# Performance work log

Measured on AMD Instinct MI355X. Metric: run time of the kernel, lower is better.

The kernel has to match this reference:

```python
import jax, jax.numpy as jnp
import numpy as np

N_NODES = 50000


def gcn_conv(h, W, b, src, dst, n_nodes):
    # PyG GCNConv: h' = D^{-1/2} (A + I) D^{-1/2} (h @ W) + b
    h = h @ W  # [N, out]
    deg = jax.ops.segment_sum(jnp.ones_like(dst, dtype=h.dtype), dst, num_segments=n_nodes)
    dinv = jnp.where(deg > 0, jax.lax.rsqrt(deg), 0.0)  # [N]
    norm = dinv[src] * dinv[dst]  # [E]
    msg = h[src] * norm[:, None]  # [E, out]
    out = jax.ops.segment_sum(msg, dst, num_segments=n_nodes)
    return out + b


def setup_inputs() -> dict:
    key = jax.random.key(0)
    ks = jax.random.split(key, 12)
    N, E, P, D, H = N_NODES, 1600000, 200000, 128, 128
    s = lambda fan_in: 1.0 / np.sqrt(fan_in)
    return {
        "x": jax.random.normal(ks[0], (N, D), dtype=jnp.float32),
        "edge_index": jax.random.randint(ks[1], (2, E), 0, N, dtype=jnp.int32),
        "drug_pairs": jax.random.randint(ks[2], (P, 2), 0, N, dtype=jnp.int32),
        "W1": jax.random.normal(ks[3], (D, H), dtype=jnp.float32) * s(D),
        "b1": jnp.zeros((H,), dtype=jnp.float32),
        "W2": jax.random.normal(ks[4], (H, H), dtype=jnp.float32) * s(H),
        "b2": jnp.zeros((H,), dtype=jnp.float32),
        "Wh1": jax.random.normal(ks[5], (2 * H, H), dtype=jnp.float32) * s(2 * H),
        "bh1": jnp.zeros((H,), dtype=jnp.float32),
        "Wh2": jax.random.normal(ks[6], (H, 1), dtype=jnp.float32) * s(H),
        "bh2": jnp.zeros((1,), dtype=jnp.float32),
    }


def reference(x, edge_index, drug_pairs, W1, b1, W2, b2, Wh1, bh1, Wh2, bh2):
    n = x.shape[0]
    # add self-loops once (GCNConv default add_self_loops=True)
    loop = jnp.arange(n, dtype=edge_index.dtype)
    src = jnp.concatenate([edge_index[0], loop])
    dst = jnp.concatenate([edge_index[1], loop])

    h = jax.nn.relu(gcn_conv(x, W1, b1, src, dst, n))  # dropout = identity (eval)
    h = jax.nn.relu(gcn_conv(h, W2, b2, src, dst, n))

    combined = jnp.concatenate([h[drug_pairs[:, 0]], h[drug_pairs[:, 1]]], axis=1)  # [P, 2H]
    out = jax.nn.relu(combined @ Wh1 + bh1) @ Wh2 + bh2  # [P, 1]
    return out
```

## Files before the change

### kernel.cpp

```cpp
#include <hip/hip_runtime.h>
#include <hip/hip_fp16.h>


#define BSH 9
#define BSZ (1 << BSH)
#define MSB 4096
#define XPAD 132
#define HB 256

typedef __attribute__((ext_vector_type(8))) short bf16x8;
typedef __attribute__((ext_vector_type(8))) _Float16 f16x8;
typedef __attribute__((ext_vector_type(4))) float f32x4;

__device__ __forceinline__ void acc8(uint4 u, float4& lo, float4& hi) {
  float2 f0 = __half22float2(((const __half2*)&u)[0]);
  float2 f1 = __half22float2(((const __half2*)&u)[1]);
  float2 f2 = __half22float2(((const __half2*)&u)[2]);
  float2 f3 = __half22float2(((const __half2*)&u)[3]);
  lo.x += f0.x; lo.y += f0.y; lo.z += f1.x; lo.w += f1.y;
  hi.x += f2.x; hi.y += f2.y; hi.z += f3.x; hi.w += f3.y;
}

__device__ __forceinline__ void split8(const float* v, bf16x8& hi, bf16x8& lo) {
#pragma unroll
  for (int j = 0; j < 8; ++j) {
    unsigned u = __float_as_uint(v[j]);
    hi[j] = (short)(u >> 16);
    float lf = v[j] - __uint_as_float(u & 0xffff0000u);
    lo[j] = (short)(__float_as_uint(lf) >> 16);
  }
}

__global__ __launch_bounds__(256) void k_prep_hist(
    const float* __restrict__ W1, const float* __restrict__ W2,
    const float* __restrict__ Wh1, short* __restrict__ fragH,
    short* __restrict__ fragL,
    const int* __restrict__ dst, int* __restrict__ gcnt, int e, int kb) {
  if (blockIdx.x >= 32) {
    __shared__ int h4[512];
    int bid = blockIdx.x - 32;
    int tid = threadIdx.x, wid = tid >> 6;
    for (int t = tid; t < 512; t += 256) h4[t] = 0;
    __syncthreads();
    for (int i = bid * 256 + tid; i < e; i += HB * 256) {
      int d = __builtin_nontemporal_load(&dst[i]);
      atomicAdd(&h4[wid * 128 + (d >> BSH)], 1);
    }
    __syncthreads();
    if (tid < kb)
      atomicAdd(&gcnt[tid], h4[tid] + h4[128 + tid] + h4[256 + tid] + h4[384 + tid]);
    return;
  }
  int g = blockIdx.x * 256 + threadIdx.x;
  int w = g >> 11;
  int rem = g & 2047;
  int lane = rem & 63;
  int ts = rem >> 6;
  int t = ts >> 2, s = ts & 3;
  int n = (t << 4) + (lane & 15);
  int k0 = s * 32 + (lane >> 4) * 8;
  const float* W = (w == 0) ? W1 : (w == 1) ? W2 : (w == 2) ? Wh1 : (Wh1 + 128 * 128);
  short h[8], l[8];
#pragma unroll
  for (int j = 0; j < 8; ++j) {
    float x = W[(k0 + j) * 128 + n];
    if (w == 0) {
      unsigned u = __float_as_uint(x);
      h[j] = (short)(u >> 16);
      float lf = x - __uint_as_float(u & 0xffff0000u);
      l[j] = (short)(__float_as_uint(lf) >> 16);
    } else {
      __half hh = __float2half(x);
      h[j] = __half_as_short(hh);
      l[j] = __half_as_short(__float2half(x - __half2float(hh)));
    }
  }
  ((int4*)fragH)[g] = *(int4*)h;
  ((int4*)fragL)[g] = *(int4*)l;
}

__device__ __forceinline__ void gemm1_body(
    const float* __restrict__ X, const short* __restrict__ fragH,
    const short* __restrict__ fragL, __half* __restrict__ C16, int n,
    int bid, float* sX) {
  int tid = threadIdx.x;
  int row0 = bid * 64;
  const float2* X2 = (const float2*)(X + (size_t)row0 * 128);
#pragma unroll
  for (int it = 0; it < 16; ++it) {
    int t = it * 256 + tid;
    int r = t >> 6, c2 = t & 63;
    int gr = row0 + r;
    float2 v = (gr < n) ? X2[t] : make_float2(0.f, 0.f);
    *(float2*)&sX[r * XPAD + c2 * 2] = v;
  }
  __syncthreads();
  int wid = tid >> 6, lane = tid & 63;
  int r0 = row0 + wid * 16;
  if (r0 >= n) return;
  int m = lane & 15, quad = lane >> 4;
  const float* xrow = sX + (wid * 16 + m) * XPAD;
  f32x4 acc[8];
#pragma unroll
  for (int t = 0; t < 8; ++t) acc[t] = (f32x4)(0.f);
  const int4* FH = (const int4*)fragH;
  const int4* FL = (const int4*)fragL;
#pragma unroll
  for (int s = 0; s < 4; ++s) {
    int k0 = s * 32 + quad * 8;
    float xv[8];
    *(float2*)&xv[0] = *(const float2*)(xrow + k0);
    *(float2*)&xv[2] = *(const float2*)(xrow + k0 + 2);
    *(float2*)&xv[4] = *(const float2*)(xrow + k0 + 4);
    *(float2*)&xv[6] = *(const float2*)(xrow + k0 + 6);
    bf16x8 ah, al;
    split8(xv, ah, al);
#pragma unroll
    for (int t = 0; t < 8; ++t) {
      int idx = (t * 4 + s) * 64 + lane;
      bf16x8 bh = *(const bf16x8*)&FH[idx];
      bf16x8 bl = *(const bf16x8*)&FL[idx];
      acc[t] = __builtin_amdgcn_mfma_f32_16x16x32_bf16(ah, bh, acc[t], 0, 0, 0);
      acc[t] = __builtin_amdgcn_mfma_f32_16x16x32_bf16(al, bh, acc[t], 0, 0, 0);
      acc[t] = __builtin_amdgcn_mfma_f32_16x16x32_bf16(ah, bl, acc[t], 0, 0, 0);
    }
  }
#pragma unroll
  for (int t = 0; t < 8; ++t) {
#pragma unroll
    for (int r = 0; r < 4; ++r) {
      int row = r0 + quad * 4 + r;
      C16[(size_t)row * 128 + t * 16 + m] = __float2half(acc[t][r]);
    }
  }
}

__device__ __forceinline__ void multisplit_body(
    const int* __restrict__ src, const int* __restrict__ dst,
    const int* __restrict__ gcnt, int* __restrict__ gcur,
    int* __restrict__ tmp, int e, int kb, int bid, int* lds) {
  int* h4 = lds;
  int* off = lds + 512;
  int* sbase = lds + 1024;
  int* ws = lds + 1152;
  int tid = threadIdx.x, wid = tid >> 6, lane = tid & 63;
  for (int t = tid; t < 512; t += 256) h4[t] = 0;
  __syncthreads();
  int i0 = bid * MSB + tid;
  int d[16], rk[16];
#pragma unroll
  for (int u = 0; u < 16; ++u) {
    int i = i0 + u * 256;
    if (i < e) {
      d[u] = __builtin_nontemporal_load(&dst[i]);
      rk[u] = atomicAdd(&h4[wid * 128 + (d[u] >> BSH)], 1);
    }
  }
  __syncthreads();
  int tot = 0;
  if (tid < 128) {
    int c0 = h4[tid], c1 = h4[128 + tid], c2 = h4[256 + tid], c3 = h4[384 + tid];
    off[tid] = 0; off[128 + tid] = c0;
    off[256 + tid] = c0 + c1; off[384 + tid] = c0 + c1 + c2;
    tot = c0 + c1 + c2 + c3;
  }
  int v = (tid < 128 && tid < kb) ? gcnt[tid] : 0;
  int orig = v;
#pragma unroll
  for (int o = 1; o < 64; o <<= 1) {
    int u = __shfl_up(v, o, 64);
    if (lane >= o) v += u;
  }
  if (lane == 63 && wid < 2) ws[wid] = v;
  __syncthreads();
  if (tid < 128) sbase[tid] = ((wid == 1) ? ws[0] : 0) + v - orig;
  __syncthreads();
  if (tid < kb && tot > 0) sbase[tid] += atomicAdd(&gcur[tid], tot);
  __syncthreads();
#pragma unroll
  for (int u = 0; u < 16; ++u) {
    int i = i0 + u * 256;
    if (i < e) {
      int s = __builtin_nontemporal_load(&src[i]);
      int k = d[u] >> BSH;
      tmp[sbase[k] + off[wid * 128 + k] + rk[u]] = ((d[u] & (BSZ - 1)) << 16) | s;
    }
  }
}

__global__ __launch_bounds__(256) void k_ms_gemm1(
    const int* __restrict__ src, const int* __restrict__ dst,
    const int* __restrict__ gcnt, int* __restrict__ gcur,
    int* __restrict__ tmp, int e, int kb, int msblocks,
    const float* __restrict__ X, const short* __restrict__ fragH,
    const short* __restrict__ fragL, __half* __restrict__ C16, int n) {
  __shared__ float sX[64 * XPAD];
  if ((int)blockIdx.x < msblocks) {
    multisplit_body(src, dst, gcnt, gcur, tmp, e, kb, blockIdx.x, (int*)sX);
    return;
  }
  gemm1_body(X, fragH, fragL, C16, n, blockIdx.x - msblocks, sX);
}

__global__ __launch_bounds__(512) void k_bucket_build(
    const int* __restrict__ tmp, const int* __restrict__ gcnt,
    int* __restrict__ rowptr, float* __restrict__ dinv,
    unsigned short* __restrict__ colarr, int n, int kb, int e) {
  __shared__ int dl[BSZ], cl[BSZ], sbase[128], ws[8];
  int t = threadIdx.x, b = blockIdx.x;
  int lane = t & 63, w = t >> 6;
  int v = (t < 128 && t < kb) ? gcnt[t] : 0;
  int orig0 = v;
#pragma unroll
  for (int o = 1; o < 64; o <<= 1) {
    int u = __shfl_up(v, o, 64);
    if (lane >= o) v += u;
  }
  if (lane == 63 && w < 2) ws[w] = v;
  dl[t] = 0;
  __syncthreads();
  if (t < 128) sbase[t] = ((w == 1) ? ws[0] : 0) + v - orig0;
  __syncthreads();
  int s0 = sbase[b];
  int s1 = s0 + gcnt[b];
  for (int j = s0 + t; j < s1; j += 512)
    atomicAdd(&dl[((unsigned)tmp[j]) >> 16], 1);
  __syncthreads();
  int dv = dl[t], orig = dv;
#pragma unroll
  for (int o = 1; o < 64; o <<= 1) {
    int u = __shfl_up(dv, o, 64);
    if (lane >= o) dv += u;
  }
  if (lane == 63) ws[w] = dv;
  __syncthreads();
  if (t == 0) {
    int a = 0;
#pragma unroll
    for (int k = 0; k < 8; ++k) { int x = ws[k]; ws[k] = a; a += x; }
  }
  __syncthreads();
  int ex = ws[w] + dv - orig;
  cl[t] = ex;
  int node = (b << BSH) + t;
  if (node < n) {
    rowptr[node] = s0 + ex;
    dinv[node] = rsqrtf((float)(orig + 1));
  }
  if (b == kb - 1 && t == 0) rowptr[n] = e;
  __syncthreads();
  for (int j = s0 + t; j < s1; j += 512) {
    int p = tmp[j];
    int r = atomicAdd(&cl[((unsigned)p) >> 16], 1);
    colarr[s0 + r] = (unsigned short)(p & 0xFFFF);
  }
}

__global__ __launch_bounds__(256) void k_gscale(__half* __restrict__ g16,
                                                const float* __restrict__ dinv,
                                                int n) {
  int idx = blockIdx.x * 256 + threadIdx.x;
  if (idx >= n * 16) return;
  float di = dinv[idx >> 4];
  uint4 u = ((const uint4*)g16)[idx];
  __half2* hp = (__half2*)&u;
#pragma unroll
  for (int k = 0; k < 4; ++k) {
    float2 f = __half22float2(hp[k]);
    hp[k] = __floats2half2_rn(f.x * di, f.y * di);
  }
  ((uint4*)g16)[idx] = u;
}

__global__ __launch_bounds__(256) void k_gemm_f16(
    const __half* __restrict__ X16, const short* __restrict__ fragH,
    const short* __restrict__ fragL, const float* __restrict__ rowscale,
    __half* __restrict__ C16, int n) {
  int wid = threadIdx.x >> 6, lane = threadIdx.x & 63;
  int r0 = (blockIdx.x * 4 + wid) * 16;
  if (r0 >= n) return;
  int m = lane & 15, quad = lane >> 4;
  const uint4* Xr = (const uint4*)(X16 + (size_t)(r0 + m) * 128);
  f32x4 acc[8];
#pragma unroll
  for (int t = 0; t < 8; ++t) acc[t] = (f32x4)(0.f);
  const int4* FH = (const int4*)fragH;
  const int4* FL = (const int4*)fragL;
#pragma unroll
  for (int s = 0; s < 4; ++s) {
    uint4 av = Xr[quad + 4 * s];
    f16x8 a = *(const f16x8*)&av;
#pragma unroll
    for (int t = 0; t < 8; ++t) {
      int idx = (t * 4 + s) * 64 + lane;
      int4 bhv = FH[idx], blv = FL[idx];
      f16x8 bh = *(const f16x8*)&bhv;
      f16x8 bl = *(const f16x8*)&blv;
      acc[t] = __builtin_amdgcn_mfma_f32_16x16x32_f16(a, bh, acc[t], 0, 0, 0);
      acc[t] = __builtin_amdgcn_mfma_f32_16x16x32_f16(a, bl, acc[t], 0, 0, 0);
    }
  }
  float sc[4];
#pragma unroll
  for (int r = 0; r < 4; ++r)
    sc[r] = rowscale ? rowscale[r0 + quad * 4 + r] : 1.f;
#pragma unroll
  for (int t = 0; t < 8; ++t) {
#pragma unroll
    for (int r = 0; r < 4; ++r) {
      int row = r0 + quad * 4 + r;
      C16[(size_t)row * 128 + t * 16 + m] = __float2half(acc[t][r] * sc[r]);
    }
  }
}

__global__ __launch_bounds__(256) void k_gemm_dual_f16(
    const __half* __restrict__ X16,
    const short* __restrict__ fHa, const short* __restrict__ fLa,
    const short* __restrict__ fHb, const short* __restrict__ fLb,
    __half* __restrict__ A16, __half* __restrict__ B16, int n) {
  int wid = threadIdx.x >> 6, lane = threadIdx.x & 63;
  int r0 = (blockIdx.x * 4 + wid) * 16;
  if (r0 >= n) return;
  int m = lane & 15, quad = lane >> 4;
  const uint4* Xr = (const uint4*)(X16 + (size_t)(r0 + m) * 128);
  f32x4 accA[8], accB[8];
#pragma unroll
  for (int t = 0; t < 8; ++t) { accA[t] = (f32x4)(0.f); accB[t] = (f32x4)(0.f); }
  const int4* FHa = (const int4*)fHa; const int4* FLa = (const int4*)fLa;
  const int4* FHb = (const int4*)fHb; const int4* FLb = (const int4*)fLb;
#pragma unroll
  for (int s = 0; s < 4; ++s) {
    uint4 av = Xr[quad + 4 * s];
    f16x8 a = *(const f16x8*)&av;
#pragma unroll
    for (int t = 0; t < 8; ++t) {
      int idx = (t * 4 + s) * 64 + lane;
      int4 v0 = FHa[idx], v1 = FLa[idx], v2 = FHb[idx], v3 = FLb[idx];
      accA[t] = __builtin_amdgcn_mfma_f32_16x16x32_f16(a, *(const f16x8*)&v0, accA[t], 0, 0, 0);
      accA[t] = __builtin_amdgcn_mfma_f32_16x16x32_f16(a, *(const f16x8*)&v1, accA[t], 0, 0, 0);
      accB[t] = __builtin_amdgcn_mfma_f32_16x16x32_f16(a, *(const f16x8*)&v2, accB[t], 0, 0, 0);
      accB[t] = __builtin_amdgcn_mfma_f32_16x16x32_f16(a, *(const f16x8*)&v3, accB[t], 0, 0, 0);
    }
  }
#pragma unroll
  for (int t = 0; t < 8; ++t) {
#pragma unroll
    for (int r = 0; r < 4; ++r) {
      int row = r0 + quad * 4 + r;
      A16[(size_t)row * 128 + t * 16 + m] = __float2half(accA[t][r]);
      B16[(size_t)row * 128 + t * 16 + m] = __float2half(accB[t][r]);
    }
  }
}

__global__ __launch_bounds__(256) void k_agg_h(
    const __half2* __restrict__ g2, const float* __restrict__ dinv,
    const int* __restrict__ rowptr, const unsigned short* __restrict__ col,
    const float* __restrict__ bias, __half* __restrict__ out16, int n) {
  int i = blockIdx.x * 4 + (threadIdx.x >> 6);
  if (i >= n) return;
  int lane = threadIdx.x & 63;
  int sub = lane >> 4;
  int c8 = lane & 15;
  const uint4* G = (const uint4*)g2;
  float4 z = make_float4(0.f, 0.f, 0.f, 0.f);
  float4 lo0 = z, lo1 = z, lo2 = z, lo3 = z, hi0 = z, hi1 = z, hi2 = z, hi3 = z;
  if (sub == 0) acc8(G[(size_t)i * 16 + c8], lo0, hi0);
  int beg = rowptr[i], end = rowptr[i + 1];
  int j = beg;
  for (; j + 16 <= end; j += 16) {
    int s0 = __builtin_nontemporal_load(&col[j + sub]);
    int s1 = __builtin_nontemporal_load(&col[j + 4 + sub]);
    int s2 = __builtin_nontemporal_load(&col[j + 8 + sub]);
    int s3 = __builtin_nontemporal_load(&col[j + 12 + sub]);
    uint4 u0 = G[(size_t)s0 * 16 + c8];
    uint4 u1 = G[(size_t)s1 * 16 + c8];
    uint4 u2 = G[(size_t)s2 * 16 + c8];
    uint4 u3 = G[(size_t)s3 * 16 + c8];
    acc8(u0, lo0, hi0); acc8(u1, lo1, hi1);
    acc8(u2, lo2, hi2); acc8(u3, lo3, hi3);
  }
  for (; j + 4 <= end; j += 4) {
    int s0 = __builtin_nontemporal_load(&col[j + sub]);
    acc8(G[(size_t)s0 * 16 + c8], lo1, hi1);
  }
  int rem = end - j;
  if (sub < rem) {
    int s0 = __builtin_nontemporal_load(&col[j + sub]);
    acc8(G[(size_t)s0 * 16 + c8], lo2, hi2);
  }
  float4 lo, hi;
  lo.x = (lo0.x + lo1.x) + (lo2.x + lo3.x);
  lo.y = (lo0.y + lo1.y) + (lo2.y + lo3.y);
  lo.z = (lo0.z + lo1.z) + (lo2.z + lo3.z);
  lo.w = (lo0.w + lo1.w) + (lo2.w + lo3.w);
  hi.x = (hi0.x + hi1.x) + (hi2.x + hi3.x);
  hi.y = (hi0.y + hi1.y) + (hi2.y + hi3.y);
  hi.z = (hi0.z + hi1.z) + (hi2.z + hi3.z);
  hi.w = (hi0.w + hi1.w) + (hi2.w + hi3.w);
  lo.x += __shfl_down(lo.x, 32, 64); lo.x += __shfl_down(lo.x, 16, 64);
  lo.y += __shfl_down(lo.y, 32, 64); lo.y += __shfl_down(lo.y, 16, 64);
  lo.z += __shfl_down(lo.z, 32, 64); lo.z += __shfl_down(lo.z, 16, 64);
  lo.w += __shfl_down(lo.w, 32, 64); lo.w += __shfl_down(lo.w, 16, 64);
  hi.x += __shfl_down(hi.x, 32, 64); hi.x += __shfl_down(hi.x, 16, 64);
  hi.y += __shfl_down(hi.y, 32, 64); hi.y += __shfl_down(hi.y, 16, 64);
  hi.z += __shfl_down(hi.z, 32, 64); hi.z += __shfl_down(hi.z, 16, 64);
  hi.w += __shfl_down(hi.w, 32, 64); hi.w += __shfl_down(hi.w, 16, 64);
  if (sub == 0) {
    float di = dinv[i];
    float4 b0 = ((const float4*)bias)[2 * c8];
    float4 b1 = ((const float4*)bias)[2 * c8 + 1];
    __half2 q0 = __floats2half2_rn(fmaxf(fmaf(di, lo.x, b0.x), 0.f),
                                   fmaxf(fmaf(di, lo.y, b0.y), 0.f));
    __half2 q1 = __floats2half2_rn(fmaxf(fmaf(di, lo.z, b0.z), 0.f),
                                   fmaxf(fmaf(di, lo.w, b0.w), 0.f));
    __half2 q2 = __floats2half2_rn(fmaxf(fmaf(di, hi.x, b1.x), 0.f),
                                   fmaxf(fmaf(di, hi.y, b1.y), 0.f));
    __half2 q3 = __floats2half2_rn(fmaxf(fmaf(di, hi.z, b1.z), 0.f),
                                   fmaxf(fmaf(di, hi.w, b1.w), 0.f));
    uint4 o;
    o.x = *(unsigned*)&q0; o.y = *(unsigned*)&q1;
    o.z = *(unsigned*)&q2; o.w = *(unsigned*)&q3;
    ((uint4*)out16)[(size_t)i * 16 + c8] = o;
  }
}

__global__ __launch_bounds__(256) void k_pairs_h(
    const __half* __restrict__ A, const __half* __restrict__ B,
    const int* __restrict__ pairs, const float* __restrict__ bh1,
    const float* __restrict__ wh2, const float* __restrict__ bh2,
    float* __restrict__ out, int P) {
  int wp = (blockIdx.x * 4 + (threadIdx.x >> 6)) * 4;
  int lane = threadIdx.x & 63;
  int sub = lane >> 4;
  int c8 = lane & 15;
  int pr = sub >> 1;
  int ab = sub & 1;
  const uint4* T = ab ? (const uint4*)B : (const uint4*)A;
  int pA = wp + pr;
  int pB = wp + 2 + pr;
  uint4 u0 = make_uint4(0, 0, 0, 0), u1 = u0;
  if (pA < P) {
    int r = pairs[2 * pA + ab];
    u0 = T[(size_t)r * 16 + c8];
  }
  if (pB < P) {
    int r = pairs[2 * pB + ab];
    u1 = T[(size_t)r * 16 + c8];
  }
  float4 b0 = ((const float4*)bh1)[2 * c8];
  float4 b1 = ((const float4*)bh1)[2 * c8 + 1];
  float4 w0 = ((const float4*)wh2)[2 * c8];
  float4 w1 = ((const float4*)wh2)[2 * c8 + 1];
  float s0, s1;
  {
    float4 lo = make_float4(0, 0, 0, 0), hi = lo;
    acc8(u0, lo, hi);
    lo.x += __shfl_down(lo.x, 16, 64); lo.y += __shfl_down(lo.y, 16, 64);
    lo.z += __shfl_down(lo.z, 16, 64); lo.w += __shfl_down(lo.w, 16, 64);
    hi.x += __shfl_down(hi.x, 16, 64); hi.y += __shfl_down(hi.y, 16, 64);
    hi.z += __shfl_down(hi.z, 16, 64); hi.w += __shfl_down(hi.w, 16, 64);
    s0 = fmaxf(lo.x + b0.x, 0.f) * w0.x + fmaxf(lo.y + b0.y, 0.f) * w0.y +
         fmaxf(lo.z + b0.z, 0.f) * w0.z + fmaxf(lo.w + b0.w, 0.f) * w0.w +
         fmaxf(hi.x + b1.x, 0.f) * w1.x + fmaxf(hi.y + b1.y, 0.f) * w1.y +
         fmaxf(hi.z + b1.z, 0.f) * w1.z + fmaxf(hi.w + b1.w, 0.f) * w1.w;
  }
  {
    float4 lo = make_float4(0, 0, 0, 0), hi = lo;
    acc8(u1, lo, hi);
    lo.x += __shfl_down(lo.x, 16, 64); lo.y += __shfl_down(lo.y, 16, 64);
    lo.z += __shfl_down(lo.z, 16, 64); lo.w += __shfl_down(lo.w, 16, 64);
    hi.x += __shfl_down(hi.x, 16, 64); hi.y += __shfl_down(hi.y, 16, 64);
    hi.z += __shfl_down(hi.z, 16, 64); hi.w += __shfl_down(hi.w, 16, 64);
    s1 = fmaxf(lo.x + b0.x, 0.f) * w0.x + fmaxf(lo.y + b0.y, 0.f) * w0.y +
         fmaxf(lo.z + b0.z, 0.f) * w0.z + fmaxf(lo.w + b0.w, 0.f) * w0.w +
         fmaxf(hi.x + b1.x, 0.f) * w1.x + fmaxf(hi.y + b1.y, 0.f) * w1.y +
         fmaxf(hi.z + b1.z, 0.f) * w1.z + fmaxf(hi.w + b1.w, 0.f) * w1.w;
  }
#pragma unroll
  for (int o = 8; o > 0; o >>= 1) {
    s0 += __shfl_down(s0, o, 64);
    s1 += __shfl_down(s1, o, 64);
  }
  float bb = bh2[0];
  if (lane == 0 && wp < P) out[wp] = s0 + bb;
  if (lane == 32 && wp + 1 < P) out[wp + 1] = s0 + bb;
  if (lane == 0 && wp + 2 < P) out[wp + 2] = s1 + bb;
  if (lane == 32 && wp + 3 < P) out[wp + 3] = s1 + bb;
}

extern "C" void kernel_launch(void* const* d_in, const int* in_sizes, int n_in,
                              void* d_out, int out_size, void* d_ws, size_t ws_size,
                              hipStream_t stream) {
  const float* x   = (const float*)d_in[0];
  const int* ei    = (const int*)d_in[1];
  const int* pairs = (const int*)d_in[2];
  const float* W1  = (const float*)d_in[3];
  const float* b1  = (const float*)d_in[4];
  const float* W2  = (const float*)d_in[5];
  const float* b2  = (const float*)d_in[6];
  const float* Wh1 = (const float*)d_in[7];
  const float* bh1 = (const float*)d_in[8];
  const float* Wh2 = (const float*)d_in[9];
  const float* bh2 = (const float*)d_in[10];
  (void)n_in; (void)out_size; (void)ws_size;

  int N = in_sizes[0] / 128;
  int E = in_sizes[1] / 2;
  int P = in_sizes[2] / 2;
  const int* src = ei;
  const int* dst = ei + E;
  int KB = (N + BSZ - 1) >> BSH;

  char* wsp = (char*)d_ws;
  size_t off = 0;
  auto alloc = [&](size_t bytes) -> void* {
    void* p = wsp + off;
    off += (bytes + 255) & ~(size_t)255;
    return p;
  };
  __half* g16 = (__half*)alloc((size_t)N * 128 * 2);
  __half* h1  = (__half*)alloc((size_t)N * 128 * 2);
  __half* h2  = (__half*)alloc((size_t)N * 128 * 2);
  float* dinv = (float*)alloc((size_t)N * 4);
  int* rowptr = (int*)alloc((size_t)(N + 1) * 4);
  unsigned short* colarr = (unsigned short*)alloc((size_t)E * 2);
  int* tmp    = (int*)alloc((size_t)E * 4);
  short* fragH = (short*)alloc(4 * 2048 * 8 * 2);
  short* fragL = (short*)alloc(4 * 2048 * 8 * 2);
  int* gc     = (int*)alloc(2 * 128 * 4);
  int* gcnt = gc;
  int* gcur = gc + 128;
  __half* A16 = g16;
  __half* B16 = h1;
  short* fH_W1 = fragH + 0 * 16384;  short* fL_W1 = fragL + 0 * 16384;
  short* fH_W2 = fragH + 1 * 16384;  short* fL_W2 = fragL + 1 * 16384;
  short* fH_Wa = fragH + 2 * 16384;  short* fL_Wa = fragL + 2 * 16384;
  short* fH_Wb = fragH + 3 * 16384;  short* fL_Wb = fragL + 3 * 16384;

  int GB = (N + 63) / 64;
  int GF = (N / 16 + 3) / 4;
  int AB = (N + 3) / 4;
  int MS = (E + MSB - 1) / MSB;

  hipMemsetAsync(gc, 0, 2 * 128 * 4, stream);
  k_prep_hist<<<32 + HB, 256, 0, stream>>>(W1, W2, Wh1, fragH, fragL,
                                           dst, gcnt, E, KB);
  k_ms_gemm1<<<MS + GB, 256, 0, stream>>>(src, dst, gcnt, gcur, tmp, E, KB, MS,
                                          x, fH_W1, fL_W1, g16, N);
  k_bucket_build<<<KB, 512, 0, stream>>>(tmp, gcnt, rowptr, dinv, colarr, N, KB, E);
  k_gscale<<<(N * 16 + 255) / 256, 256, 0, stream>>>(g16, dinv, N);
  k_agg_h<<<AB, 256, 0, stream>>>((const __half2*)g16, dinv, rowptr, colarr, b1, h1, N);
  k_gemm_f16<<<GF, 256, 0, stream>>>(h1, fH_W2, fL_W2, dinv, g16, N);
  k_agg_h<<<AB, 256, 0, stream>>>((const __half2*)g16, dinv, rowptr, colarr, b2, h2, N);
  k_gemm_dual_f16<<<GF, 256, 0, stream>>>(h2, fH_Wa, fL_Wa, fH_Wb, fL_Wb,
                                          A16, B16, N);
  k_pairs_h<<<(P + 15) / 16, 256, 0, stream>>>(A16, B16, pairs, bh1, Wh2, bh2,
                                               (float*)d_out, P);
}
```

Baseline: 344.9 us.

## Fuse row scaling into bucket build and unroll histogram loops

Removes the separate k_gscale launch by applying the dinv scaling of g16 inside k_bucket_build, using per-block degree values kept in shared memory. The dst histogram now reads four ints per vector load with a 2x unrolled stride. The bucket count and scatter loops are unrolled 8x so more independent loads are in flight. This saves one launch and one global read of dinv, but the 98-block bucket kernel now also carries the whole g16 scaling pass, which may serialize work that was previously spread across many blocks.

```diff
diff --git a/kernel.cpp b/kernel.cpp
--- a/kernel.cpp
+++ b/kernel.cpp
@@ -11,6 +11,7 @@
 typedef __attribute__((ext_vector_type(8))) short bf16x8;
 typedef __attribute__((ext_vector_type(8))) _Float16 f16x8;
 typedef __attribute__((ext_vector_type(4))) float f32x4;
+typedef __attribute__((ext_vector_type(4))) int i32x4;
 
 __device__ __forceinline__ void acc8(uint4 u, float4& lo, float4& hi) {
   float2 f0 = __half22float2(((const __half2*)&u)[0]);
@@ -42,8 +43,31 @@
     int tid = threadIdx.x, wid = tid >> 6;
     for (int t = tid; t < 512; t += 256) h4[t] = 0;
     __syncthreads();
-    for (int i = bid * 256 + tid; i < e; i += HB * 256) {
-      int d = __builtin_nontemporal_load(&dst[i]);
+    const i32x4* dst4 = (const i32x4*)dst;
+    int ne4 = e >> 2;
+    const int STR = HB * 256;
+    int i = bid * 256 + tid;
+    for (; i < ne4 - STR; i += 2 * STR) {
+      i32x4 a = __builtin_nontemporal_load(&dst4[i]);
+      i32x4 b = __builtin_nontemporal_load(&dst4[i + STR]);
+      atomicAdd(&h4[wid * 128 + (a.x >> BSH)], 1);
+      atomicAdd(&h4[wid * 128 + (a.y >> BSH)], 1);
+      atomicAdd(&h4[wid * 128 + (a.z >> BSH)], 1);
+      atomicAdd(&h4[wid * 128 + (a.w >> BSH)], 1);
+      atomicAdd(&h4[wid * 128 + (b.x >> BSH)], 1);
+      atomicAdd(&h4[wid * 128 + (b.y >> BSH)], 1);
+      atomicAdd(&h4[wid * 128 + (b.z >> BSH)], 1);
+      atomicAdd(&h4[wid * 128 + (b.w >> BSH)], 1);
+    }
+    for (; i < ne4; i += STR) {
+      i32x4 a = __builtin_nontemporal_load(&dst4[i]);
+      atomicAdd(&h4[wid * 128 + (a.x >> BSH)], 1);
+      atomicAdd(&h4[wid * 128 + (a.y >> BSH)], 1);
+      atomicAdd(&h4[wid * 128 + (a.z >> BSH)], 1);
+      atomicAdd(&h4[wid * 128 + (a.w >> BSH)], 1);
+    }
+    if (bid == 0 && tid < (e & 3)) {
+      int d = dst[(ne4 << 2) + tid];
       atomicAdd(&h4[wid * 128 + (d >> BSH)], 1);
     }
     __syncthreads();
@@ -205,8 +229,10 @@
 __global__ __launch_bounds__(512) void k_bucket_build(
     const int* __restrict__ tmp, const int* __restrict__ gcnt,
     int* __restrict__ rowptr, float* __restrict__ dinv,
-    unsigned short* __restrict__ colarr, int n, int kb, int e) {
+    unsigned short* __restrict__ colarr, __half* __restrict__ g16,
+    int n, int kb, int e) {
   __shared__ int dl[BSZ], cl[BSZ], sbase[128], ws[8];
+  __shared__ float sdi[BSZ];
   int t = threadIdx.x, b = blockIdx.x;
   int lane = t & 63, w = t >> 6;
   int v = (t < 128 && t < kb) ? gcnt[t] : 0;
@@ -223,8 +249,29 @@
   __syncthreads();
   int s0 = sbase[b];
   int s1 = s0 + gcnt[b];
-  for (int j = s0 + t; j < s1; j += 512)
-    atomicAdd(&dl[((unsigned)tmp[j]) >> 16], 1);
+  {
+    int j = s0 + t;
+    for (; j < s1 - 3584; j += 4096) {
+      int v0 = tmp[j];
+      int v1 = tmp[j + 512];
+      int v2 = tmp[j + 1024];
+      int v3 = tmp[j + 1536];
+      int v4 = tmp[j + 2048];
+      int v5 = tmp[j + 2560];
+      int v6 = tmp[j + 3072];
+      int v7 = tmp[j + 3584];
+      atomicAdd(&dl[((unsigned)v0) >> 16], 1);
+      atomicAdd(&dl[((unsigned)v1) >> 16], 1);
+      atomicAdd(&dl[((unsigned)v2) >> 16], 1);
+      atomicAdd(&dl[((unsigned)v3) >> 16], 1);
+      atomicAdd(&dl[((unsigned)v4) >> 16], 1);
+      atomicAdd(&dl[((unsigned)v5) >> 16], 1);
+      atomicAdd(&dl[((unsigned)v6) >> 16], 1);
+      atomicAdd(&dl[((unsigned)v7) >> 16], 1);
+    }
+    for (; j < s1; j += 512)
+      atomicAdd(&dl[((unsigned)tmp[j]) >> 16], 1);
+  }
   __syncthreads();
   int dv = dl[t], orig = dv;
 #pragma unroll
@@ -243,33 +290,67 @@
   int ex = ws[w] + dv - orig;
   cl[t] = ex;
   int node = (b << BSH) + t;
+  float di = rsqrtf((float)(orig + 1));
+  sdi[t] = di;
   if (node < n) {
     rowptr[node] = s0 + ex;
-    dinv[node] = rsqrtf((float)(orig + 1));
+    dinv[node] = di;
   }
   if (b == kb - 1 && t == 0) rowptr[n] = e;
   __syncthreads();
-  for (int j = s0 + t; j < s1; j += 512) {
-    int p = tmp[j];
-    int r = atomicAdd(&cl[((unsigned)p) >> 16], 1);
-    colarr[s0 + r] = (unsigned short)(p & 0xFFFF);
-  }
-}
-
-__global__ __launch_bounds__(256) void k_gscale(__half* __restrict__ g16,
-                                                const float* __restrict__ dinv,
-                                                int n) {
-  int idx = blockIdx.x * 256 + threadIdx.x;
-  if (idx >= n * 16) return;
-  float di = dinv[idx >> 4];
-  uint4 u = ((const uint4*)g16)[idx];
-  __half2* hp = (__half2*)&u;
-#pragma unroll
-  for (int k = 0; k < 4; ++k) {
-    float2 f = __half22float2(hp[k]);
-    hp[k] = __floats2half2_rn(f.x * di, f.y * di);
-  }
-  ((uint4*)g16)[idx] = u;
+  {
+    int j = s0 + t;
+    for (; j < s1 - 3584; j += 4096) {
+      int p0 = tmp[j];
+      int p1 = tmp[j + 512];
+      int p2 = tmp[j + 1024];
+      int p3 = tmp[j + 1536];
+      int p4 = tmp[j + 2048];
+      int p5 = tmp[j + 2560];
+      int p6 = tmp[j + 3072];
+      int p7 = tmp[j + 3584];
+      int r0 = atomicAdd(&cl[((unsigned)p0) >> 16], 1);
+      int r1 = atomicAdd(&cl[((unsigned)p1) >> 16], 1);
+      int r2 = atomicAdd(&cl[((unsigned)p2) >> 16], 1);
+      int r3 = atomicAdd(&cl[((unsigned)p3) >> 16], 1);
+      int r4 = atomicAdd(&cl[((unsigned)p4) >> 16], 1);
+      int r5 = atomicAdd(&cl[((unsigned)p5) >> 16], 1);
+      int r6 = atomicAdd(&cl[((unsigned)p6) >> 16], 1);
+      int r7 = atomicAdd(&cl[((unsigned)p7) >> 16], 1);
+      colarr[s0 + r0] = (unsigned short)(p0 & 0xFFFF);
+      colarr[s0 + r1] = (unsigned short)(p1 & 0xFFFF);
+      colarr[s0 + r2] = (unsigned short)(p2 & 0xFFFF);
+      colarr[s0 + r3] = (unsigned short)(p3 & 0xFFFF);
+      colarr[s0 + r4] = (unsigned short)(p4 & 0xFFFF);
+      colarr[s0 + r5] = (unsigned short)(p5 & 0xFFFF);
+      colarr[s0 + r6] = (unsigned short)(p6 & 0xFFFF);
+      colarr[s0 + r7] = (unsigned short)(p7 & 0xFFFF);
+    }
+    for (; j < s1; j += 512) {
+      int p = tmp[j];
+      int r = atomicAdd(&cl[((unsigned)p) >> 16], 1);
+      colarr[s0 + r] = (unsigned short)(p & 0xFFFF);
+    }
+  }
+  {
+    int base = b << BSH;
+    int rows = n - base;
+    if (rows > BSZ) rows = BSZ;
+    uint4* G = (uint4*)g16;
+    for (int idx = t; idx < rows * 16; idx += 512) {
+      int rl = idx >> 4;
+      float dsc = sdi[rl];
+      size_t gi = (size_t)(base + rl) * 16 + (idx & 15);
+      uint4 u = G[gi];
+      __half2* hp = (__half2*)&u;
+#pragma unroll
+      for (int k2 = 0; k2 < 4; ++k2) {
+        float2 f = __half22float2(hp[k2]);
+        hp[k2] = __floats2half2_rn(f.x * dsc, f.y * dsc);
+      }
+      G[gi] = u;
+    }
+  }
 }
 
 __global__ __launch_bounds__(256) void k_gemm_f16(
@@ -549,8 +630,8 @@
                                            dst, gcnt, E, KB);
   k_ms_gemm1<<<MS + GB, 256, 0, stream>>>(src, dst, gcnt, gcur, tmp, E, KB, MS,
                                           x, fH_W1, fL_W1, g16, N);
-  k_bucket_build<<<KB, 512, 0, stream>>>(tmp, gcnt, rowptr, dinv, colarr, N, KB, E);
-  k_gscale<<<(N * 16 + 255) / 256, 256, 0, stream>>>(g16, dinv, N);
+  k_bucket_build<<<KB, 512, 0, stream>>>(tmp, gcnt, rowptr, dinv, colarr,
+                                         g16, N, KB, E);
   k_agg_h<<<AB, 256, 0, stream>>>((const __half2*)g16, dinv, rowptr, colarr, b1, h1, N);
   k_gemm_f16<<<GF, 256, 0, stream>>>(h1, fH_W2, fL_W2, dinv, g16, N);
   k_agg_h<<<AB, 256, 0, stream>>>((const __half2*)g16, dinv, rowptr, colarr, b2, h2, N);
```

New measurement: 336.4 us. 2.5% less time.
